# Performance work log

Hardware: AMD Instinct MI355X
Metric: run time of the kernel (lower is better)

## Reference

```python
import jax, jax.numpy as jnp
import numpy as np

B, T, C = 2, 4096, 512
H = 8
D = C // H  # head_dim = 64


def setup_inputs() -> dict:
    key = jax.random.key(0)
    ks = jax.random.split(key, 9)
    s = 0.02
    return {
        "x": jax.random.normal(ks[0], (B, T, C), dtype=jnp.float32),
        "wq": jax.random.normal(ks[1], (C, C), dtype=jnp.float32) * s,
        "bq": jnp.zeros((C,), dtype=jnp.float32),
        "wk": jax.random.normal(ks[2], (C, C), dtype=jnp.float32) * s,
        "bk": jnp.zeros((C,), dtype=jnp.float32),
        "wv": jax.random.normal(ks[3], (C, C), dtype=jnp.float32) * s,
        "bv": jnp.zeros((C,), dtype=jnp.float32),
        "wo": jax.random.normal(ks[4], (C, C), dtype=jnp.float32) * s,
        "bo": jnp.zeros((C,), dtype=jnp.float32),
    }


def reference(x, wq, bq, wk, bk, wv, bv, wo, bo):
    Bx, Tx, Cx = x.shape
    # projections: y = x @ W^T + b (torch Linear convention: W is [out, in])
    q = (x @ wq.T + bq).reshape(Bx, Tx, H, D).transpose(0, 2, 1, 3)  # [B,H,T,D]
    k = (x @ wk.T + bk).reshape(Bx, Tx, H, D).transpose(0, 2, 1, 3)
    v = (x @ wv.T + bv).reshape(Bx, Tx, H, D).transpose(0, 2, 1, 3)
    scores = jnp.einsum("bhqd,bhkd->bhqk", q, k) * (D ** -0.5)  # [B,H,T,T]
    causal = jnp.tril(jnp.ones((Tx, Tx), dtype=bool))
    scores = jnp.where(causal, scores, -jnp.inf)
    weights = jax.nn.softmax(scores, axis=-1)
    o = jnp.einsum("bhqk,bhkd->bhqd", weights, v)  # [B,H,T,D]
    o = o.transpose(0, 2, 1, 3).reshape(Bx, Tx, Cx)
    return o @ wo.T + bo
```

## Files before the change

kernel.cpp:

```cpp
#include <hip/hip_runtime.h>
#include <math.h>

static constexpr int Bb = 2;
static constexpr int Tt = 4096;
static constexpr int Cc = 512;
static constexpr int Hh = 8;
static constexpr int Dd = 64;
static constexpr int Mtot = Bb * Tt;

#define QSCALE 0.1803368801111f
#define NTICK 1024

typedef __attribute__((ext_vector_type(8)))  short   short8;
typedef __attribute__((ext_vector_type(4)))  float   f32x4;
typedef __attribute__((ext_vector_type(16))) float   f32x16;
typedef __attribute__((ext_vector_type(4)))  unsigned int   uint4v;
typedef __attribute__((ext_vector_type(4)))  unsigned short ushort4v;

__device__ inline unsigned short f2bf(float f) {
    unsigned int u = __float_as_uint(f);
    u += 0x7fffu + ((u >> 16) & 1u);
    return (unsigned short)(u >> 16);
}
__device__ inline float bf2f(unsigned short u) {
    return __uint_as_float((unsigned int)u << 16);
}

__device__ inline unsigned int cvtpk_bf16(float a, float b) {
    unsigned int r;
    asm("v_cvt_pk_bf16_f32 %0, %1, %2" : "=v"(r) : "v"(a), "v"(b));
    return r;
}

__device__ inline int SW(int row) { return (row ^ (row >> 3)) & 7; }

__device__ inline void gload16(const void* g, void* lds) {
    __builtin_amdgcn_global_load_lds(
        (const __attribute__((address_space(1))) void*)g,
        (__attribute__((address_space(3))) void*)lds, 16, 0, 0);
}

__global__ __launch_bounds__(256)
void cast_all(const float* __restrict__ x,
              const float* __restrict__ w0, const float* __restrict__ w1,
              const float* __restrict__ w2, const float* __restrict__ w3,
              unsigned short* __restrict__ xb, unsigned short* __restrict__ wb,
              int* __restrict__ ctr) {
    const int bid = (int)blockIdx.x;
    if (bid == 0 && threadIdx.x == 0) *ctr = 0;
    const float* src;
    unsigned short* dst;
    size_t i;
    if (bid < 2048) {
        src = x; dst = xb;
        i = ((size_t)bid * 256 + threadIdx.x) * 8;
    } else {
        const float* srcs[4] = {w0, w1, w2, w3};
        const int wi = (bid - 2048) >> 7;
        src = srcs[wi];
        dst = wb + (size_t)wi * (Cc * Cc);
        i = ((size_t)((bid - 2048) & 127) * 256 + threadIdx.x) * 8;
    }
    const float4 a = *reinterpret_cast<const float4*>(src + i);
    const float4 b = *reinterpret_cast<const float4*>(src + i + 4);
    short8 o;
    o[0] = (short)f2bf(a.x); o[1] = (short)f2bf(a.y);
    o[2] = (short)f2bf(a.z); o[3] = (short)f2bf(a.w);
    o[4] = (short)f2bf(b.x); o[5] = (short)f2bf(b.y);
    o[6] = (short)f2bf(b.z); o[7] = (short)f2bf(b.w);
    *reinterpret_cast<short8*>(dst + i) = o;
}

__global__ __launch_bounds__(256)
void proj_qkv(const unsigned short* __restrict__ A, const unsigned short* __restrict__ Wall,
              const float* __restrict__ bq, const float* __restrict__ bk,
              const float* __restrict__ bv,
              unsigned short* __restrict__ qo, unsigned short* __restrict__ ko,
              unsigned short* __restrict__ vo) {
    __shared__ unsigned short As[128][32];
    __shared__ unsigned short Bs[128][32];

    const int which = blockIdx.z;
    const unsigned short* Wb = Wall + (size_t)which * Cc * Cc;
    const float* bias = (which == 0) ? bq : (which == 1) ? bk : bv;
    unsigned short* outp = (which == 0) ? qo : (which == 1) ? ko : vo;
    const float scale = (which == 0) ? QSCALE : 1.0f;

    const int tid = threadIdx.x;
    const int lane = tid & 63;
    const int w = tid >> 6;
    const int wr = w >> 1, wc = w & 1;
    const int l15 = lane & 15, lg = lane >> 4;
    const int m0 = blockIdx.x * 128, n0 = blockIdx.y * 128;

    f32x4 acc[4][4] = {};

    for (int k0 = 0; k0 < Cc; k0 += 32) {
        #pragma unroll
        for (int i = 0; i < 2; ++i) {
            const int idx = tid + i * 256;
            const int row = idx >> 2, g = idx & 3;
            *reinterpret_cast<short8*>(&As[row][g * 8]) =
                *reinterpret_cast<const short8*>(&A[(size_t)(m0 + row) * Cc + k0 + g * 8]);
            *reinterpret_cast<short8*>(&Bs[row][g * 8]) =
                *reinterpret_cast<const short8*>(&Wb[(size_t)(n0 + row) * Cc + k0 + g * 8]);
        }
        __syncthreads();
        short8 a[4], b[4];
        #pragma unroll
        for (int mi = 0; mi < 4; ++mi)
            a[mi] = *reinterpret_cast<const short8*>(&As[wr * 64 + mi * 16 + l15][lg * 8]);
        #pragma unroll
        for (int nj = 0; nj < 4; ++nj)
            b[nj] = *reinterpret_cast<const short8*>(&Bs[wc * 64 + nj * 16 + l15][lg * 8]);
        #pragma unroll
        for (int mi = 0; mi < 4; ++mi)
            #pragma unroll
            for (int nj = 0; nj < 4; ++nj)
                acc[mi][nj] = __builtin_amdgcn_mfma_f32_16x16x32_bf16(a[mi], b[nj], acc[mi][nj], 0, 0, 0);
        __syncthreads();
    }

    #pragma unroll
    for (int mi = 0; mi < 4; ++mi) {
        #pragma unroll
        for (int nj = 0; nj < 4; ++nj) {
            const int col = n0 + wc * 64 + nj * 16 + l15;
            const float bvv = bias[col];
            if (which == 2) {
                const int mbase = m0 + wr * 64 + mi * 16 + lg * 4;
                const int b_ = mbase >> 12, t = mbase & (Tt - 1);
                const int h = col >> 6, d = col & 63;
                ushort4v o;
                #pragma unroll
                for (int r = 0; r < 4; ++r)
                    o[r] = f2bf(acc[mi][nj][r] + bvv);
                *reinterpret_cast<ushort4v*>(
                    &outp[(((size_t)b_ * Hh + h) * Dd + d) * Tt + t]) = o;
            } else {
                #pragma unroll
                for (int r = 0; r < 4; ++r) {
                    const int row = m0 + wr * 64 + mi * 16 + lg * 4 + r;
                    const int b_ = row >> 12, t = row & (Tt - 1);
                    const int h = col >> 6, d = col & 63;
                    outp[(((size_t)b_ * Hh + h) * Tt + t) * Dd + d] =
                        f2bf((acc[mi][nj][r] + bvv) * scale);
                }
            }
        }
    }
}

__global__ __launch_bounds__(256)
void proj_out(const unsigned short* __restrict__ opart, const float* __restrict__ lp,
              const unsigned short* __restrict__ Wb,
              const float* __restrict__ bias, float* __restrict__ outp) {
    __shared__ unsigned short As[64][32];
    __shared__ unsigned short Bs[128][32];

    const int tid = threadIdx.x;
    const int lane = tid & 63;
    const int w = tid >> 6;
    const int l15 = lane & 15, lg = lane >> 4;
    const int m0 = blockIdx.x * 64, n0 = blockIdx.y * 128;

    const int row_a = tid >> 2;
    const int sg = tid & 3;
    const int m = m0 + row_a;
    const int b_a = m >> 12, t_a = m & (Tt - 1);
    const size_t cs = (size_t)16 * Tt;

    const int srow = (w << 4) + (lane >> 2);
    const int sgb = lane & 3;

    f32x4 acc[4][2] = {};

    for (int k0 = 0; k0 < Cc; k0 += 32) {
        {
            const int c0 = k0 + sg * 8;
            const int h = c0 >> 6, d0 = c0 & 63;
            const size_t rbase = ((size_t)b_a * Hh + h) * Tt + t_a;
            const float lsum = lp[rbase] + lp[cs + rbase] +
                               lp[2 * cs + rbase] + lp[3 * cs + rbase];
            const float inv = 1.f / lsum;
            float s[8] = {};
            #pragma unroll
            for (int chk = 0; chk < 4; ++chk) {
                const short8 v8 = *reinterpret_cast<const short8*>(
                    &opart[(chk * cs + rbase) * 64 + d0]);
                #pragma unroll
                for (int e = 0; e < 8; ++e) s[e] += bf2f((unsigned short)v8[e]);
            }
            short8 o8;
            #pragma unroll
            for (int e = 0; e < 8; ++e) o8[e] = (short)f2bf(s[e] * inv);
            *reinterpret_cast<short8*>(&As[row_a][((sg ^ (row_a & 3))) * 8]) = o8;
        }
        #pragma unroll
        for (int i = 0; i < 2; ++i) {
            const int row = 64 * i + srow;
            const int gc = (sgb ^ (row & 3)) * 8;
            gload16(&Wb[(size_t)(n0 + row) * Cc + k0 + gc], &Bs[64 * i + (w << 4)][0]);
        }
        __syncthreads();

        short8 a[4], b[2];
        const int rg = (lg ^ (l15 & 3)) * 8;
        #pragma unroll
        for (int mi = 0; mi < 4; ++mi)
            a[mi] = *reinterpret_cast<const short8*>(&As[mi * 16 + l15][rg]);
        #pragma unroll
        for (int nj = 0; nj < 2; ++nj)
            b[nj] = *reinterpret_cast<const short8*>(&Bs[w * 32 + nj * 16 + l15][rg]);
        #pragma unroll
        for (int mi = 0; mi < 4; ++mi)
            #pragma unroll
            for (int nj = 0; nj < 2; ++nj)
                acc[mi][nj] = __builtin_amdgcn_mfma_f32_16x16x32_bf16(a[mi], b[nj], acc[mi][nj], 0, 0, 0);
        __syncthreads();
    }

    #pragma unroll
    for (int mi = 0; mi < 4; ++mi) {
        #pragma unroll
        for (int nj = 0; nj < 2; ++nj) {
            const int col = n0 + w * 32 + nj * 16 + l15;
            const float bv = bias[col];
            #pragma unroll
            for (int r = 0; r < 4; ++r) {
                const int row = m0 + mi * 16 + lg * 4 + r;
                outp[(size_t)row * Cc + col] = acc[mi][nj][r] + bv;
            }
        }
    }
}

__global__ __launch_bounds__(512)
void attn_mfma(const unsigned short* __restrict__ qb, const unsigned short* __restrict__ kb,
               const unsigned short* __restrict__ vtb,
               unsigned short* __restrict__ opart, float* __restrict__ lp,
               int* __restrict__ ctr) {
    __shared__ unsigned short Ks[3][64][64];
    __shared__ unsigned short Vts[3][64][64];
    __shared__ int tkt;

    const int tid = threadIdx.x;
    const int w = tid >> 6;
    const int lane = tid & 63;
    const int l31 = lane & 31, hi = lane >> 5;

    const int r0 = (w << 3) + (lane >> 3);
    const int gk0 = ((lane & 7) ^ SW(r0)) * 8;

    for (;;) {
        __syncthreads();
        if (tid == 0) tkt = atomicAdd(ctr, 1);
        __syncthreads();
        const int t = tkt;
        if (t >= NTICK) break;

        const int qt = 15 - (t >> 6);
        const int ch = (t >> 4) & 3;
        const int bh = t & 15;
        const int t0 = (qt + 1) * ch;
        const int t1 = (qt + 1) * (ch + 1);

        const int qg = qt * 256 + w * 32 + l31;

        short8 qf[4];
        {
            const unsigned short* qp = qb + ((size_t)bh * Tt + qg) * Dd + hi * 8;
            #pragma unroll
            for (int sl = 0; sl < 4; ++sl)
                qf[sl] = *reinterpret_cast<const short8*>(qp + sl * 16);
        }

        const unsigned short* kb_h = kb + (size_t)bh * Tt * Dd;
        const unsigned short* vt_h = vtb + (size_t)bh * Dd * Tt;

        auto STAGE = [&](int kt_, int slot) {
            const int n64 = kt_ * 64;
            gload16(kb_h + (size_t)(n64 + r0) * Dd + gk0, &Ks[slot][(w << 3)][0]);
            gload16(vt_h + (size_t)r0 * Tt + n64 + gk0, &Vts[slot][(w << 3)][0]);
        };

        f32x16 oacc[2] = {};
        float lrow = 0.f;

        const int qmax_w = qt * 256 + w * 32 + 31;
        const int qmin_w = qt * 256 + w * 32;

        STAGE(t0, 0);
        if (t0 + 1 < t1) STAGE(t0 + 1, 1);

        int cur = 0;
        for (int kt = t0; kt < t1; ++kt) {
            if (kt + 1 < t1) {
                asm volatile("s_waitcnt vmcnt(2)" ::: "memory");
            } else {
                asm volatile("s_waitcnt vmcnt(0)" ::: "memory");
            }
            __builtin_amdgcn_s_barrier();
            __builtin_amdgcn_sched_barrier(0);

            if (kt + 2 < t1) {
                const int stg = (cur + 2 >= 3) ? (cur - 1) : (cur + 2);
                STAGE(kt + 2, stg);
            }

            if (kt * 64 <= qmax_w) {
                f32x16 sacc[2];
                __builtin_amdgcn_s_setprio(1);
                #pragma unroll
                for (int f = 0; f < 2; ++f) {
                    f32x16 z = {};
                    const int krow = f * 32 + l31;
                    const int sw = SW(krow);
                    #pragma unroll
                    for (int sl = 0; sl < 4; ++sl) {
                        const short8 kf = *reinterpret_cast<const short8*>(
                            &Ks[cur][krow][((2 * sl + hi) ^ sw) * 8]);
                        z = __builtin_amdgcn_mfma_f32_32x32x16_bf16(kf, qf[sl], z, 0, 0, 0);
                    }
                    sacc[f] = z;
                }
                __builtin_amdgcn_s_setprio(0);

                if (kt * 64 + 63 > qmin_w) {
                    #pragma unroll
                    for (int f = 0; f < 2; ++f)
                        #pragma unroll
                        for (int r = 0; r < 16; ++r) {
                            const int kvg = kt * 64 + f * 32 + (r & 3) + 8 * (r >> 2) + 4 * hi;
                            if (kvg > qg) sacc[f][r] = -INFINITY;
                        }
                }

                #pragma unroll
                for (int f = 0; f < 2; ++f)
                    #pragma unroll
                    for (int r = 0; r < 16; ++r)
                        sacc[f][r] = exp2f(sacc[f][r]);

                float t16[16];
                #pragma unroll
                for (int r = 0; r < 16; ++r) t16[r] = sacc[0][r] + sacc[1][r];
                #pragma unroll
                for (int r = 0; r < 8; ++r) t16[r] += t16[r + 8];
                #pragma unroll
                for (int r = 0; r < 4; ++r) t16[r] += t16[r + 4];
                t16[0] += t16[2];
                t16[1] += t16[3];
                lrow += t16[0] + t16[1];

                #pragma unroll
                for (int f = 0; f < 2; ++f) {
                    #pragma unroll
                    for (int s2 = 0; s2 < 2; ++s2) {
                        const int b0 = s2 * 8;
                        unsigned int c01 = cvtpk_bf16(sacc[f][b0 + 0], sacc[f][b0 + 1]);
                        unsigned int c23 = cvtpk_bf16(sacc[f][b0 + 2], sacc[f][b0 + 3]);
                        unsigned int c45 = cvtpk_bf16(sacc[f][b0 + 4], sacc[f][b0 + 5]);
                        unsigned int c67 = cvtpk_bf16(sacc[f][b0 + 6], sacc[f][b0 + 7]);
                        asm("v_permlane32_swap_b32 %0, %1" : "+v"(c01), "+v"(c45));
                        asm("v_permlane32_swap_b32 %0, %1" : "+v"(c23), "+v"(c67));
                        uint4v paw;
                        paw[0] = c01; paw[1] = c23; paw[2] = c45; paw[3] = c67;
                        const short8 pa = *reinterpret_cast<short8*>(&paw);
                        const int g = 4 * f + 2 * s2;
                        __builtin_amdgcn_s_setprio(1);
                        #pragma unroll
                        for (int nb = 0; nb < 2; ++nb) {
                            const int vrow = nb * 32 + l31;
                            const short8 vf = *reinterpret_cast<const short8*>(
                                &Vts[cur][vrow][((g + hi) ^ SW(vrow)) * 8]);
                            oacc[nb] = __builtin_amdgcn_mfma_f32_32x32x16_bf16(pa, vf, oacc[nb], 0, 0, 0);
                        }
                        __builtin_amdgcn_s_setprio(0);
                    }
                }
            }

            cur = (cur == 2) ? 0 : cur + 1;
        }

        const float lf = lrow + __shfl_xor(lrow, 32);
        const size_t pbase = ((size_t)ch * 16 + bh) * Tt;
        if (hi == 0) lp[pbase + qg] = lf;
        #pragma unroll
        for (int r = 0; r < 16; ++r) {
            const int qr = (r & 3) + 8 * (r >> 2) + 4 * hi;
            const int tg = qt * 256 + w * 32 + qr;
            unsigned short* dst = opart + (pbase + tg) * 64 + l31;
            dst[0]  = f2bf(oacc[0][r]);
            dst[32] = f2bf(oacc[1][r]);
        }
    }
}

extern "C" void kernel_launch(void* const* d_in, const int* in_sizes, int n_in,
                              void* d_out, int out_size, void* d_ws, size_t ws_size,
                              hipStream_t stream) {
    const float* x  = (const float*)d_in[0];
    const float* wq = (const float*)d_in[1];
    const float* bq = (const float*)d_in[2];
    const float* wk = (const float*)d_in[3];
    const float* bk = (const float*)d_in[4];
    const float* wv = (const float*)d_in[5];
    const float* bv = (const float*)d_in[6];
    const float* wo = (const float*)d_in[7];
    const float* bo = (const float*)d_in[8];
    float* out = (float*)d_out;

    const size_t nTok = (size_t)Mtot * Cc;
    const size_t nW   = (size_t)Cc * Cc;

    unsigned short* xb    = (unsigned short*)d_ws;
    unsigned short* wqb   = xb + nTok;
    unsigned short* wob   = wqb + 3 * nW;
    unsigned short* qbuf  = wqb + 4 * nW;
    unsigned short* kbuf  = qbuf + nTok;
    unsigned short* vtbuf = kbuf + nTok;
    unsigned short* opart = vtbuf + nTok;
    float* lp  = (float*)(opart + (size_t)4 * 16 * Tt * 64);
    int*   ctr = (int*)(lp + (size_t)4 * 16 * Tt);

    cast_all<<<dim3(2560), 256, 0, stream>>>(x, wq, wk, wv, wo, xb, wqb, ctr);

    proj_qkv<<<dim3(Mtot / 128, Cc / 128, 3), 256, 0, stream>>>(
        xb, wqb, bq, bk, bv, qbuf, kbuf, vtbuf);

    attn_mfma<<<dim3(512), 512, 0, stream>>>(qbuf, kbuf, vtbuf, opart, lp, ctr);

    proj_out<<<dim3(Mtot / 64, Cc / 128), 256, 0, stream>>>(opart, lp, wob, bo, out);
}
```

Before: 141.8 us.

## Double K-step in QKV projection and split attention PV accumulators

In the QKV projection GEMM, each iteration now loads a K-chunk of 64 instead of 32, with padded LDS rows (72). This halves the number of barrier pairs and makes each sync cover more MFMA work. In the attention kernel, the PV accumulation is split into two independent accumulator sets, one per score fragment, which are summed at the end. The row-sum reduction is reorganized per fragment. The aim is to break the serial MFMA dependency chain and let exp/convert work on one fragment overlap with MFMAs on the other. The cost is more registers, which may lower occupancy, plus a larger LDS footprint.

After: 138.9 us (median of 2 runs). -2.1%, faster.

```diff
diff --git a/kernel.cpp b/kernel.cpp
--- a/kernel.cpp
+++ b/kernel.cpp
@@ -77,8 +77,8 @@
               const float* __restrict__ bv,
               unsigned short* __restrict__ qo, unsigned short* __restrict__ ko,
               unsigned short* __restrict__ vo) {
-    __shared__ unsigned short As[128][32];
-    __shared__ unsigned short Bs[128][32];
+    __shared__ unsigned short As[128][72];
+    __shared__ unsigned short Bs[128][72];
 
     const int which = blockIdx.z;
     const unsigned short* Wb = Wall + (size_t)which * Cc * Cc;
@@ -95,29 +95,34 @@
 
     f32x4 acc[4][4] = {};
 
-    for (int k0 = 0; k0 < Cc; k0 += 32) {
-        #pragma unroll
-        for (int i = 0; i < 2; ++i) {
+    for (int k0 = 0; k0 < Cc; k0 += 64) {
+        #pragma unroll
+        for (int i = 0; i < 4; ++i) {
             const int idx = tid + i * 256;
-            const int row = idx >> 2, g = idx & 3;
+            const int row = idx >> 3, g = idx & 7;
             *reinterpret_cast<short8*>(&As[row][g * 8]) =
                 *reinterpret_cast<const short8*>(&A[(size_t)(m0 + row) * Cc + k0 + g * 8]);
             *reinterpret_cast<short8*>(&Bs[row][g * 8]) =
                 *reinterpret_cast<const short8*>(&Wb[(size_t)(n0 + row) * Cc + k0 + g * 8]);
         }
         __syncthreads();
-        short8 a[4], b[4];
-        #pragma unroll
-        for (int mi = 0; mi < 4; ++mi)
-            a[mi] = *reinterpret_cast<const short8*>(&As[wr * 64 + mi * 16 + l15][lg * 8]);
-        #pragma unroll
-        for (int nj = 0; nj < 4; ++nj)
-            b[nj] = *reinterpret_cast<const short8*>(&Bs[wc * 64 + nj * 16 + l15][lg * 8]);
-        #pragma unroll
-        for (int mi = 0; mi < 4; ++mi)
+        #pragma unroll
+        for (int kh = 0; kh < 2; ++kh) {
+            short8 a[4], b[4];
+            #pragma unroll
+            for (int mi = 0; mi < 4; ++mi)
+                a[mi] = *reinterpret_cast<const short8*>(
+                    &As[wr * 64 + mi * 16 + l15][kh * 32 + lg * 8]);
             #pragma unroll
             for (int nj = 0; nj < 4; ++nj)
-                acc[mi][nj] = __builtin_amdgcn_mfma_f32_16x16x32_bf16(a[mi], b[nj], acc[mi][nj], 0, 0, 0);
+                b[nj] = *reinterpret_cast<const short8*>(
+                    &Bs[wc * 64 + nj * 16 + l15][kh * 32 + lg * 8]);
+            #pragma unroll
+            for (int mi = 0; mi < 4; ++mi)
+                #pragma unroll
+                for (int nj = 0; nj < 4; ++nj)
+                    acc[mi][nj] = __builtin_amdgcn_mfma_f32_16x16x32_bf16(a[mi], b[nj], acc[mi][nj], 0, 0, 0);
+        }
         __syncthreads();
     }
 
@@ -284,7 +289,8 @@
             gload16(vt_h + (size_t)r0 * Tt + n64 + gk0, &Vts[slot][(w << 3)][0]);
         };
 
-        f32x16 oacc[2] = {};
+        f32x16 oaccA[2] = {};
+        f32x16 oaccB[2] = {};
         float lrow = 0.f;
 
         const int qmax_w = qt * 256 + w * 32 + 31;
@@ -337,24 +343,21 @@
                 }
 
                 #pragma unroll
-                for (int f = 0; f < 2; ++f)
+                for (int f = 0; f < 2; ++f) {
                     #pragma unroll
                     for (int r = 0; r < 16; ++r)
                         sacc[f][r] = exp2f(sacc[f][r]);
 
-                float t16[16];
-                #pragma unroll
-                for (int r = 0; r < 16; ++r) t16[r] = sacc[0][r] + sacc[1][r];
-                #pragma unroll
-                for (int r = 0; r < 8; ++r) t16[r] += t16[r + 8];
-                #pragma unroll
-                for (int r = 0; r < 4; ++r) t16[r] += t16[r + 4];
-                t16[0] += t16[2];
-                t16[1] += t16[3];
-                lrow += t16[0] + t16[1];
-
-                #pragma unroll
-                for (int f = 0; f < 2; ++f) {
+                    float t8[8];
+                    #pragma unroll
+                    for (int r = 0; r < 8; ++r) t8[r] = sacc[f][r] + sacc[f][r + 8];
+                    #pragma unroll
+                    for (int r = 0; r < 4; ++r) t8[r] += t8[r + 4];
+                    t8[0] += t8[2];
+                    t8[1] += t8[3];
+                    lrow += t8[0] + t8[1];
+
+                    f32x16* oacc = (f == 0) ? oaccA : oaccB;
                     #pragma unroll
                     for (int s2 = 0; s2 < 2; ++s2) {
                         const int b0 = s2 * 8;
@@ -392,8 +395,8 @@
             const int qr = (r & 3) + 8 * (r >> 2) + 4 * hi;
             const int tg = qt * 256 + w * 32 + qr;
             unsigned short* dst = opart + (pbase + tg) * 64 + l31;
-            dst[0]  = f2bf(oacc[0][r]);
-            dst[32] = f2bf(oacc[1][r]);
+            dst[0]  = f2bf(oaccA[0][r] + oaccB[0][r]);
+            dst[32] = f2bf(oaccA[1][r] + oaccB[1][r]);
         }
     }
 }
```
